# Performance work log

Hardware: AMD Instinct MI355X
Metric: run time of the kernel (lower is better)

The kernel has to match this reference:

```python
import jax, jax.numpy as jnp
import numpy as np
from jax import lax

N, C, H, W = 32, 256, 56, 56
SHIFT = 2  # p_5_1_0, frozen random.randint(-3,3)

def setup_inputs() -> dict:
    key = jax.random.key(0)
    k1, k2, k3 = jax.random.split(key, 3)
    x = jax.random.normal(k1, (N, C, H, W), dtype=jnp.float32)
    w6 = jax.random.normal(k2, (C, 1), dtype=jnp.float32) * 0.1  # trunc_normal(std=0.1) approx
    w7 = jax.random.normal(k3, (C, C * 25), dtype=jnp.float32) * (1.0 / np.sqrt(C * 25))
    return {"x": x, "w6": w6, "w7": w7}

def reference(x, w6, w7):
    # t_1: max over width -> (n,c,h)
    t1 = jnp.max(x, axis=3)
    # t_3/t_4: relu then tanh
    t4 = jnp.tanh(jax.nn.relu(x))
    # t_5: roll along height axis
    t5 = jnp.roll(x, SHIFT, axis=2)
    # t_6: einsum 'abcd,be->aecd' with e=1 -> (n,h,w)
    t6 = jnp.einsum('nchw,c->nhw', t4, w6[:, 0])
    # t_2 + p_7: unfold(5x5, dilation=3, padding=6) + 1x1 conv == dilated 5x5 conv.
    # unfold channel ordering is c*25 + (kh*5+kw), so reshape to OIHW directly.
    conv_w = w7.reshape(C, C, 5, 5)
    t7 = lax.conv_general_dilated(
        x, conv_w, window_strides=(1, 1), padding=[(6, 6), (6, 6)],
        rhs_dilation=(3, 3), dimension_numbers=('NCHW', 'OIHW', 'NCHW'))
    t8 = x * t7
    # t_9: softmax over width of (n,h,w)
    t9 = jax.nn.softmax(t6, axis=2)
    t10 = t9[:, None, :, :] * t5
    t11 = t10 + t8
    return t1[:, :, :, None] - t11
```

## Files before the change

kernel.cpp:

```cpp
#include <hip/hip_runtime.h>
#include <hip/hip_bf16.h>
#include <math.h>

typedef __bf16 bf16x8 __attribute__((ext_vector_type(8)));
typedef short  s16x8  __attribute__((ext_vector_type(8)));
typedef float  f32x16 __attribute__((ext_vector_type(16)));
typedef unsigned short u16;

#define NN 32
#define CC 256
#define HH 56
#define WW 56
#define HP 68
#define XP2_BYTES 75759616ull
#define XP2_OFF 0ull
#define WT3_OFF 75759616ull
#define T1_OFF  79036416ull
#define T9_OFF  80871424ull

__device__ inline u16 f2bf(float f) {
    unsigned int u = __builtin_bit_cast(unsigned int, f);
    u = (u + 0x7fffu + ((u >> 16) & 1u)) >> 16;
    return (u16)u;
}

__device__ inline void gl_lds16(const char* g, char* l) {
    __builtin_amdgcn_global_load_lds(
        (const __attribute__((address_space(1))) unsigned int*)g,
        (__attribute__((address_space(3))) unsigned int*)l, 16, 0, 0);
}

__global__ void zero_halo(u16* __restrict__ xp2) {
    const int total = NN * 1488 * 32;
    int i = blockIdx.x * blockDim.x + threadIdx.x;
    const int stride = gridDim.x * blockDim.x;
    uint4 z; z.x = z.y = z.z = z.w = 0u;
    for (; i < total; i += stride) {
        int chunk = i & 31;
        int pid = i >> 5;
        int n = pid / 1488;
        int hp = pid - n * 1488;
        int row, col;
        if (hp < 816) { int r = hp / 68; col = hp - r * 68; row = (r < 6) ? r : r + 56; }
        else { int hq = hp - 816; int rr = hq / 12; int c12 = hq - rr * 12;
               row = 6 + rr; col = (c12 < 6) ? c12 : c12 + 56; }
        *(uint4*)((char*)xp2 + ((((size_t)n * HP + row) * HP + col) * 512) + chunk * 16) = z;
    }
}

__global__ __launch_bounds__(256)
void pack_w(const float* __restrict__ w7, u16* __restrict__ wt3) {
    int idx = blockIdx.x * 256 + threadIdx.x;
    int c_out = idx / 6400;
    int k = idx - c_out * 6400;
    int cin = k / 25;
    int tap = k - cin * 25;
    int kn = tap * 8 + (cin >> 5);
    int c5 = cin & 31;
    int ks = c5 >> 4, half = (c5 >> 3) & 1, j = c5 & 7;
    int lane = half * 32 + (c_out & 31);
    int rb = c_out >> 5;
    wt3[(size_t)kn * 8192 + ks * 4096 + rb * 512 + lane * 8 + j] = f2bf(w7[idx]);
}

__global__ __launch_bounds__(256)
void prep(const float* __restrict__ x, const float* __restrict__ w6,
          float* __restrict__ t1, float* __restrict__ t9,
          u16* __restrict__ xp2) {
    const int n = blockIdx.x / HH;
    const int h = blockIdx.x % HH;
    const int lane = threadIdx.x & 63;
    const int wid = threadIdx.x >> 6;
    const bool valid = lane < WW;
    const int wl = valid ? lane : (WW - 1);
    __shared__ u16 xbuf[64 * 66];
    __shared__ float sbuf[4 * 64];
    const float* xrow = x + ((size_t)(n * CC) * HH + h) * WW;
    u16* dst = xp2 + (((size_t)n * HP + h + 6) * HP + 6) * CC;
    float accw = 0.f;
    for (int g = 0; g < 4; ++g) {
        if (g) __syncthreads();
        const int c0 = g * 64 + wid * 16;
#pragma unroll
        for (int r0 = 0; r0 < 16; r0 += 4) {
            float xv0 = xrow[(size_t)(c0 + r0 + 0) * (HH * WW) + wl];
            float xv1 = xrow[(size_t)(c0 + r0 + 1) * (HH * WW) + wl];
            float xv2 = xrow[(size_t)(c0 + r0 + 2) * (HH * WW) + wl];
            float xv3 = xrow[(size_t)(c0 + r0 + 3) * (HH * WW) + wl];
            if (valid) {
                xbuf[(wid * 16 + r0 + 0) * 66 + lane] = f2bf(xv0);
                xbuf[(wid * 16 + r0 + 1) * 66 + lane] = f2bf(xv1);
                xbuf[(wid * 16 + r0 + 2) * 66 + lane] = f2bf(xv2);
                xbuf[(wid * 16 + r0 + 3) * 66 + lane] = f2bf(xv3);
            }
            float m0 = valid ? xv0 : -INFINITY;
            float m1 = valid ? xv1 : -INFINITY;
            float m2 = valid ? xv2 : -INFINITY;
            float m3 = valid ? xv3 : -INFINITY;
#pragma unroll
            for (int off = 32; off > 0; off >>= 1) {
                m0 = fmaxf(m0, __shfl_xor(m0, off));
                m1 = fmaxf(m1, __shfl_xor(m1, off));
                m2 = fmaxf(m2, __shfl_xor(m2, off));
                m3 = fmaxf(m3, __shfl_xor(m3, off));
            }
            if (lane == 0) {
                t1[(size_t)(n * CC + c0 + r0 + 0) * HH + h] = m0;
                t1[(size_t)(n * CC + c0 + r0 + 1) * HH + h] = m1;
                t1[(size_t)(n * CC + c0 + r0 + 2) * HH + h] = m2;
                t1[(size_t)(n * CC + c0 + r0 + 3) * HH + h] = m3;
            }
            if (valid) {
                float e0 = __expf(2.f * fmaxf(xv0, 0.f));
                float e1 = __expf(2.f * fmaxf(xv1, 0.f));
                float e2 = __expf(2.f * fmaxf(xv2, 0.f));
                float e3 = __expf(2.f * fmaxf(xv3, 0.f));
                accw += (1.f - 2.f * __builtin_amdgcn_rcpf(e0 + 1.f)) * w6[c0 + r0 + 0];
                accw += (1.f - 2.f * __builtin_amdgcn_rcpf(e1 + 1.f)) * w6[c0 + r0 + 1];
                accw += (1.f - 2.f * __builtin_amdgcn_rcpf(e2 + 1.f)) * w6[c0 + r0 + 2];
                accw += (1.f - 2.f * __builtin_amdgcn_rcpf(e3 + 1.f)) * w6[c0 + r0 + 3];
            }
        }
        __syncthreads();
        for (int id = threadIdx.x; id < WW * 8; id += 256) {
            int p = id >> 3, ch8 = id & 7;
            s16x8 pk;
#pragma unroll
            for (int j = 0; j < 8; ++j)
                pk[j] = (short)xbuf[(ch8 * 8 + j) * 66 + p];
            *(s16x8*)(dst + (size_t)p * CC + g * 64 + ch8 * 8) = pk;
        }
    }
    sbuf[wid * 64 + lane] = accw;
    __syncthreads();
    if (wid == 0) {
        float s = sbuf[lane] + sbuf[64 + lane] + sbuf[128 + lane] + sbuf[192 + lane];
        float sm = valid ? s : -INFINITY;
        float mx = sm;
#pragma unroll
        for (int off = 32; off > 0; off >>= 1)
            mx = fmaxf(mx, __shfl_xor(mx, off));
        float e = valid ? expf(s - mx) : 0.f;
        float tot = e;
#pragma unroll
        for (int off = 32; off > 0; off >>= 1)
            tot += __shfl_xor(tot, off);
        if (valid) t9[((size_t)n * HH + h) * WW + lane] = e / tot;
    }
}

__global__ __launch_bounds__(512, 2)
void conv_main(const char* __restrict__ xp2b, const char* __restrict__ wt3b,
               const float* __restrict__ x, const float* __restrict__ t1,
               const float* __restrict__ t9, float* __restrict__ out) {
    extern __shared__ __align__(16) char smem[];
    const int bid = blockIdx.x;
    const int tile = (bid & 7) * 49 + (bid >> 3);
    const int tid  = threadIdx.x;
    const int wid  = tid >> 6;
    const int lane = tid & 63;
    const int l31 = lane & 31;
    const int lhi = lane >> 5;
    const int wr = wid >> 2;
    const int wc = wid & 3;

    unsigned vb;
    {
        int p = tile * 256 + wid * 32 + l31;
        int n = p / (HH * WW);
        int rem = p - n * (HH * WW);
        int hh = rem / WW;
        int ww = rem - hh * WW;
        vb = ((((unsigned)n * HP + hh + 6) * HP) + ww + 6) * 512 + lhi * 16;
    }

    auto stageA = [&](int tt, int ks) {
        const int kn = (tt < 200) ? tt : (tt - 200);
        const unsigned o = ks * 8192 + wid * 1024 + lane * 16;
        char* d = smem + (size_t)(tt & 3) * 32768 + o;
        const char* g = wt3b + (size_t)kn * 16384 + o;
        gl_lds16(g, d);
    };
    auto stageB = [&](int tt, int ks) {
        const int kn = (tt < 200) ? tt : (tt - 200);
        const int tp = kn >> 3, ch = kn & 7;
        const char* gb = xp2b +
            (ptrdiff_t)((tp / 5) * 3 - 6) * (HP * 512) +
            (ptrdiff_t)((tp % 5) * 3 - 6) * 512 + ch * 64 + ks * 32 + vb;
        char* d = smem + (size_t)(tt & 3) * 32768 + 16384
                  + ks * 8192 + wid * 1024 + lane * 16;
        gl_lds16(gb, d);
    };

    f32x16 acc[4][2];
#pragma unroll
    for (int mi = 0; mi < 4; ++mi)
#pragma unroll
        for (int nb = 0; nb < 2; ++nb)
#pragma unroll
            for (int r = 0; r < 16; ++r)
                acc[mi][nb][r] = 0.f;

    const int aoff = wr * 4096 + lane * 16;
    const int boff = 16384 + wc * 2048 + lane * 16;

#pragma unroll
    for (int tt = 0; tt < 3; ++tt) {
        stageA(tt, 0); stageB(tt, 0);
        stageA(tt, 1); stageB(tt, 1);
    }
    asm volatile("s_waitcnt vmcnt(8)" ::: "memory");
    __builtin_amdgcn_s_barrier();

    for (int tb = 0; tb < 200; tb += 4) {
#pragma unroll
        for (int u = 0; u < 4; ++u) {
            const int t = tb + u;
            const char* bp = smem + (size_t)u * 32768;
            stageA(t + 3, 0); stageB(t + 3, 0);
            stageA(t + 3, 1); stageB(t + 3, 1);
            bf16x8 av[4], bv[2];
#pragma unroll
            for (int ks = 0; ks < 2; ++ks) {
#pragma unroll
                for (int nb = 0; nb < 2; ++nb)
                    bv[nb] = *(const bf16x8*)(const void*)(bp + boff + ks * 8192 + nb * 1024);
#pragma unroll
                for (int mi = 0; mi < 4; ++mi)
                    av[mi] = *(const bf16x8*)(const void*)(bp + aoff + ks * 8192 + mi * 1024);
                __builtin_amdgcn_s_setprio(1);
#pragma unroll
                for (int mi = 0; mi < 4; ++mi)
#pragma unroll
                    for (int nb = 0; nb < 2; ++nb)
                        acc[mi][nb] = __builtin_amdgcn_mfma_f32_32x32x16_bf16(
                            av[mi], bv[nb], acc[mi][nb], 0, 0, 0);
                __builtin_amdgcn_s_setprio(0);
            }
            asm volatile("s_waitcnt vmcnt(8)" ::: "memory");
            __builtin_amdgcn_s_barrier();
        }
    }

#pragma unroll
    for (int nb = 0; nb < 2; ++nb) {
        const int p = tile * 256 + wc * 64 + nb * 32 + l31;
        const int n = p / (HH * WW);
        const int rem = p - n * (HH * WW);
        const int h = rem / WW;
        const int w = rem - h * WW;
        const float t9v = t9[((size_t)n * HH + h) * WW + w];
        const int hprev = (h >= 2) ? (h - 2) : (h + HH - 2);
#pragma unroll
        for (int mi = 0; mi < 4; ++mi) {
            const int c0 = wr * 128 + mi * 32 + 4 * lhi;
#pragma unroll
            for (int r = 0; r < 16; ++r) {
                const int c = c0 + (r & 3) + 8 * (r >> 2);
                const size_t rowi = (size_t)(n * CC + c) * HH;
                const float t1v = t1[rowi + h];
                const float xv = x[(rowi + h) * WW + w];
                const float xr = x[(rowi + hprev) * WW + w];
                out[(rowi + h) * WW + w] = t1v - (t9v * xr + xv * acc[mi][nb][r]);
            }
        }
    }
}

extern "C" void kernel_launch(void* const* d_in, const int* in_sizes, int n_in,
                              void* d_out, int out_size, void* d_ws, size_t ws_size,
                              hipStream_t stream) {
    const float* x  = (const float*)d_in[0];
    const float* w6 = (const float*)d_in[1];
    const float* w7 = (const float*)d_in[2];
    float* out = (float*)d_out;
    char* ws = (char*)d_ws;
    u16*   xp2 = (u16*)(ws + XP2_OFF);
    u16*   wt3 = (u16*)(ws + WT3_OFF);
    float* t1  = (float*)(ws + T1_OFF);
    float* t9  = (float*)(ws + T9_OFF);

    static bool lds_cfg_done = false;
    if (!lds_cfg_done) {
        (void)hipFuncSetAttribute((const void*)conv_main,
                                  hipFuncAttributeMaxDynamicSharedMemorySize,
                                  131072);
        lds_cfg_done = true;
    }

    zero_halo<<<dim3(1024), dim3(256), 0, stream>>>(xp2);
    pack_w<<<dim3(6400), dim3(256), 0, stream>>>(w7, wt3);
    prep<<<dim3(NN * HH), dim3(256), 0, stream>>>(x, w6, t1, t9, xp2);
    conv_main<<<dim3(392), dim3(512), 131072, stream>>>((const char*)xp2, (const char*)wt3,
                                                        x, t1, t9, out);
}
```

Baseline: 629.8 us.

## Vectorize prep loads with float4 and interleave conv staging per k-step

The prep kernel now has each lane read four contiguous width elements with float4 loads, so 16 lanes cover a row. The width max reduces over 16 lanes instead of 64, and the tanh-weighted partial sums go through a 16x56 shared buffer. The conv main loop drops its 4x manual unroll and issues the async staging for tile t+3 split per ks half, interleaved with the MFMA work, so loads spread across the compute. This may change how the compiler schedules the loads against the MFMAs and adds loop overhead.

```diff
diff --git a/kernel.cpp b/kernel.cpp
--- a/kernel.cpp
+++ b/kernel.cpp
@@ -4,6 +4,7 @@
 
 typedef __bf16 bf16x8 __attribute__((ext_vector_type(8)));
 typedef short  s16x8  __attribute__((ext_vector_type(8)));
+typedef short  s16x4  __attribute__((ext_vector_type(4)));
 typedef float  f32x16 __attribute__((ext_vector_type(16)));
 typedef unsigned short u16;
 
@@ -69,72 +70,67 @@
           u16* __restrict__ xp2) {
     const int n = blockIdx.x / HH;
     const int h = blockIdx.x % HH;
-    const int lane = threadIdx.x & 63;
-    const int wid = threadIdx.x >> 6;
-    const bool valid = lane < WW;
-    const int wl = valid ? lane : (WW - 1);
-    __shared__ u16 xbuf[64 * 66];
-    __shared__ float sbuf[4 * 64];
+    const int tid = threadIdx.x;
+    const int lane = tid & 63;
+    const int wid = tid >> 6;
+    const int g16 = lane >> 4;
+    const int wq  = lane & 15;
+    const bool act = wq < 14;
+    __shared__ u16 xbuf[64 * 60];
+    __shared__ float sacc[16][56];
     const float* xrow = x + ((size_t)(n * CC) * HH + h) * WW;
     u16* dst = xp2 + (((size_t)n * HP + h + 6) * HP + 6) * CC;
-    float accw = 0.f;
+    float a0 = 0.f, a1 = 0.f, a2 = 0.f, a3 = 0.f;
     for (int g = 0; g < 4; ++g) {
         if (g) __syncthreads();
-        const int c0 = g * 64 + wid * 16;
-#pragma unroll
-        for (int r0 = 0; r0 < 16; r0 += 4) {
-            float xv0 = xrow[(size_t)(c0 + r0 + 0) * (HH * WW) + wl];
-            float xv1 = xrow[(size_t)(c0 + r0 + 1) * (HH * WW) + wl];
-            float xv2 = xrow[(size_t)(c0 + r0 + 2) * (HH * WW) + wl];
-            float xv3 = xrow[(size_t)(c0 + r0 + 3) * (HH * WW) + wl];
-            if (valid) {
-                xbuf[(wid * 16 + r0 + 0) * 66 + lane] = f2bf(xv0);
-                xbuf[(wid * 16 + r0 + 1) * 66 + lane] = f2bf(xv1);
-                xbuf[(wid * 16 + r0 + 2) * 66 + lane] = f2bf(xv2);
-                xbuf[(wid * 16 + r0 + 3) * 66 + lane] = f2bf(xv3);
+#pragma unroll
+        for (int it = 0; it < 4; ++it) {
+            const int cl = wid * 16 + it * 4 + g16;
+            const int c  = g * 64 + cl;
+            float4 v = make_float4(0.f, 0.f, 0.f, 0.f);
+            if (act) v = *(const float4*)(xrow + (size_t)c * (HH * WW) + wq * 4);
+            if (act) {
+                s16x4 pk;
+                pk[0] = (short)f2bf(v.x); pk[1] = (short)f2bf(v.y);
+                pk[2] = (short)f2bf(v.z); pk[3] = (short)f2bf(v.w);
+                *(s16x4*)(xbuf + cl * 60 + wq * 4) = pk;
             }
-            float m0 = valid ? xv0 : -INFINITY;
-            float m1 = valid ? xv1 : -INFINITY;
-            float m2 = valid ? xv2 : -INFINITY;
-            float m3 = valid ? xv3 : -INFINITY;
-#pragma unroll
-            for (int off = 32; off > 0; off >>= 1) {
-                m0 = fmaxf(m0, __shfl_xor(m0, off));
-                m1 = fmaxf(m1, __shfl_xor(m1, off));
-                m2 = fmaxf(m2, __shfl_xor(m2, off));
-                m3 = fmaxf(m3, __shfl_xor(m3, off));
+            float m = act ? fmaxf(fmaxf(v.x, v.y), fmaxf(v.z, v.w)) : -INFINITY;
+#pragma unroll
+            for (int off = 8; off > 0; off >>= 1)
+                m = fmaxf(m, __shfl_xor(m, off));
+            if (wq == 0) t1[(size_t)(n * CC + c) * HH + h] = m;
+            if (act) {
+                const float wc = w6[c];
+                a0 += wc * (1.f - 2.f * __builtin_amdgcn_rcpf(__expf(2.f * fmaxf(v.x, 0.f)) + 1.f));
+                a1 += wc * (1.f - 2.f * __builtin_amdgcn_rcpf(__expf(2.f * fmaxf(v.y, 0.f)) + 1.f));
+                a2 += wc * (1.f - 2.f * __builtin_amdgcn_rcpf(__expf(2.f * fmaxf(v.z, 0.f)) + 1.f));
+                a3 += wc * (1.f - 2.f * __builtin_amdgcn_rcpf(__expf(2.f * fmaxf(v.w, 0.f)) + 1.f));
             }
-            if (lane == 0) {
-                t1[(size_t)(n * CC + c0 + r0 + 0) * HH + h] = m0;
-                t1[(size_t)(n * CC + c0 + r0 + 1) * HH + h] = m1;
-                t1[(size_t)(n * CC + c0 + r0 + 2) * HH + h] = m2;
-                t1[(size_t)(n * CC + c0 + r0 + 3) * HH + h] = m3;
-            }
-            if (valid) {
-                float e0 = __expf(2.f * fmaxf(xv0, 0.f));
-                float e1 = __expf(2.f * fmaxf(xv1, 0.f));
-                float e2 = __expf(2.f * fmaxf(xv2, 0.f));
-                float e3 = __expf(2.f * fmaxf(xv3, 0.f));
-                accw += (1.f - 2.f * __builtin_amdgcn_rcpf(e0 + 1.f)) * w6[c0 + r0 + 0];
-                accw += (1.f - 2.f * __builtin_amdgcn_rcpf(e1 + 1.f)) * w6[c0 + r0 + 1];
-                accw += (1.f - 2.f * __builtin_amdgcn_rcpf(e2 + 1.f)) * w6[c0 + r0 + 2];
-                accw += (1.f - 2.f * __builtin_amdgcn_rcpf(e3 + 1.f)) * w6[c0 + r0 + 3];
-            }
         }
         __syncthreads();
-        for (int id = threadIdx.x; id < WW * 8; id += 256) {
+        for (int id = tid; id < WW * 8; id += 256) {
             int p = id >> 3, ch8 = id & 7;
             s16x8 pk;
 #pragma unroll
             for (int j = 0; j < 8; ++j)
-                pk[j] = (short)xbuf[(ch8 * 8 + j) * 66 + p];
+                pk[j] = (short)xbuf[(ch8 * 8 + j) * 60 + p];
             *(s16x8*)(dst + (size_t)p * CC + g * 64 + ch8 * 8) = pk;
         }
     }
-    sbuf[wid * 64 + lane] = accw;
+    if (act) {
+        float* sl = sacc[wid * 4 + g16];
+        sl[wq * 4 + 0] = a0; sl[wq * 4 + 1] = a1;
+        sl[wq * 4 + 2] = a2; sl[wq * 4 + 3] = a3;
+    }
     __syncthreads();
     if (wid == 0) {
-        float s = sbuf[lane] + sbuf[64 + lane] + sbuf[128 + lane] + sbuf[192 + lane];
+        const bool valid = lane < WW;
+        float s = 0.f;
+        if (valid) {
+#pragma unroll
+            for (int gi = 0; gi < 16; ++gi) s += sacc[gi][lane];
+        }
         float sm = valid ? s : -INFINITY;
         float mx = sm;
 #pragma unroll
@@ -212,34 +208,30 @@
     asm volatile("s_waitcnt vmcnt(8)" ::: "memory");
     __builtin_amdgcn_s_barrier();
 
-    for (int tb = 0; tb < 200; tb += 4) {
-#pragma unroll
-        for (int u = 0; u < 4; ++u) {
-            const int t = tb + u;
-            const char* bp = smem + (size_t)u * 32768;
-            stageA(t + 3, 0); stageB(t + 3, 0);
-            stageA(t + 3, 1); stageB(t + 3, 1);
-            bf16x8 av[4], bv[2];
-#pragma unroll
-            for (int ks = 0; ks < 2; ++ks) {
+    for (int t = 0; t < 200; ++t) {
+        const char* bp = smem + (size_t)(t & 3) * 32768;
+        bf16x8 av[4], bv[2];
+
+#pragma unroll
+        for (int ks = 0; ks < 2; ++ks) {
+            stageA(t + 3, ks); stageB(t + 3, ks);
+#pragma unroll
+            for (int nb = 0; nb < 2; ++nb)
+                bv[nb] = *(const bf16x8*)(const void*)(bp + boff + ks * 8192 + nb * 1024);
+#pragma unroll
+            for (int mi = 0; mi < 4; ++mi)
+                av[mi] = *(const bf16x8*)(const void*)(bp + aoff + ks * 8192 + mi * 1024);
+            __builtin_amdgcn_s_setprio(1);
+#pragma unroll
+            for (int mi = 0; mi < 4; ++mi)
 #pragma unroll
                 for (int nb = 0; nb < 2; ++nb)
-                    bv[nb] = *(const bf16x8*)(const void*)(bp + boff + ks * 8192 + nb * 1024);
-#pragma unroll
-                for (int mi = 0; mi < 4; ++mi)
-                    av[mi] = *(const bf16x8*)(const void*)(bp + aoff + ks * 8192 + mi * 1024);
-                __builtin_amdgcn_s_setprio(1);
-#pragma unroll
-                for (int mi = 0; mi < 4; ++mi)
-#pragma unroll
-                    for (int nb = 0; nb < 2; ++nb)
-                        acc[mi][nb] = __builtin_amdgcn_mfma_f32_32x32x16_bf16(
-                            av[mi], bv[nb], acc[mi][nb], 0, 0, 0);
-                __builtin_amdgcn_s_setprio(0);
-            }
-            asm volatile("s_waitcnt vmcnt(8)" ::: "memory");
-            __builtin_amdgcn_s_barrier();
-        }
+                    acc[mi][nb] = __builtin_amdgcn_mfma_f32_32x32x16_bf16(
+                        av[mi], bv[nb], acc[mi][nb], 0, 0, 0);
+            __builtin_amdgcn_s_setprio(0);
+        }
+        asm volatile("s_waitcnt vmcnt(8)" ::: "memory");
+        __builtin_amdgcn_s_barrier();
     }
 
 #pragma unroll
```

Measured after the change: 585.9 us. 7.0% less time.
